# Optimization experiments

Measured on AMD Instinct MI355X. Metric: run time of the kernel, lower is better.

## Reference

```python
import jax, jax.numpy as jnp
import numpy as np

INPUT_DIM = 1024
DIM_K = 512
DIM_V = 512
N = 8192  # query rows
M = 8192  # key/value rows


def setup_inputs() -> dict:
    key = jax.random.key(0)
    ks = jax.random.split(key, 9)
    s_in = 1.0 / np.sqrt(INPUT_DIM)
    return {
        "q": jax.random.normal(ks[0], (N, INPUT_DIM), jnp.float32),
        "k": jax.random.normal(ks[1], (M, INPUT_DIM), jnp.float32),
        "v": jax.random.normal(ks[2], (M, INPUT_DIM), jnp.float32),
        "Wq": jax.random.normal(ks[3], (DIM_K, INPUT_DIM), jnp.float32) * s_in,
        "bq": jax.random.normal(ks[4], (DIM_K,), jnp.float32) * s_in,
        "Wk": jax.random.normal(ks[5], (DIM_K, INPUT_DIM), jnp.float32) * s_in,
        "bk": jax.random.normal(ks[6], (DIM_K,), jnp.float32) * s_in,
        "Wv": jax.random.normal(ks[7], (DIM_V, INPUT_DIM), jnp.float32) * s_in,
        "bv": jax.random.normal(ks[8], (DIM_V,), jnp.float32) * s_in,
    }


def reference(q, k, v, Wq, bq, Wk, bk, Wv, bv):
    norm_fact = 1.0 / np.sqrt(DIM_K).astype(np.float32)
    Q = q @ Wq.T + bq  # [N, dim_k]
    K = k @ Wk.T + bk  # [M, dim_k]
    V = v @ Wv.T + bv  # [M, dim_v]
    scores = Q @ K.T  # [N, M]
    # NOTE: faithful to source — scale is applied AFTER softmax
    atten = jax.nn.softmax(scores, axis=-1) * norm_fact
    return atten @ V  # [N, dim_v]
```

## Files before the change

### kernel.cpp

```cpp
#include <hip/hip_runtime.h>
#include <hip/hip_bf16.h>

#define IN_DIM 1024
#define DK 512
#define DV 512
#define NQ 8192
#define NKV 8192

typedef _Float16 f16x8 __attribute__((ext_vector_type(8)));
typedef _Float16 f16x4 __attribute__((ext_vector_type(4)));
typedef float f32x4 __attribute__((ext_vector_type(4)));

__global__ __launch_bounds__(256, 2) void proj_kernel(
    const float* __restrict__ qin, const float* __restrict__ kin, const float* __restrict__ vin,
    const float* __restrict__ Wq, const float* __restrict__ bq,
    const float* __restrict__ Wk, const float* __restrict__ bk,
    const float* __restrict__ Wv, const float* __restrict__ bv,
    _Float16* __restrict__ Qp, _Float16* __restrict__ Kp, _Float16* __restrict__ Vp)
{
    const int z = blockIdx.z;
    const float* A  = (z == 0) ? qin : (z == 1) ? kin : vin;
    const float* W  = (z == 0) ? Wq  : (z == 1) ? Wk  : Wv;
    const float* bi = (z == 0) ? bq  : (z == 1) ? bk  : bv;

    __shared__ __align__(16) char psm[73728];
    _Float16 (*As)[128][72] = (_Float16(*)[128][72])psm;
    _Float16 (*Bs)[128][72] = (_Float16(*)[128][72])(psm + 36864);
    _Float16* trans = (_Float16*)psm;

    const int tid = threadIdx.x;
    const int rowbase = blockIdx.y * 128;
    const int colbase = blockIdx.x * 128;
    const int wave = tid >> 6;
    const int lane = tid & 63;
    const int quad = lane >> 4;
    const int l16  = lane & 15;
    const int wrow = (wave & 1) * 64;
    const int wcol = (wave >> 1) * 64;

    float4 ra[8], rb[8];
    auto ld = [&](int kc) {
#pragma unroll
        for (int i = 0; i < 8; ++i) {
            int idx = tid + i * 256;
            int row = idx >> 4, c4 = idx & 15;
            ra[i] = *(const float4*)&A[(size_t)(rowbase + row) * IN_DIM + kc * 64 + c4 * 4];
            rb[i] = *(const float4*)&W[(size_t)(colbase + row) * IN_DIM + kc * 64 + c4 * 4];
        }
    };
    auto st = [&](int buf) {
#pragma unroll
        for (int i = 0; i < 8; ++i) {
            int idx = tid + i * 256;
            int row = idx >> 4, c4 = idx & 15;
            f16x4 pa, pb;
            pa[0] = (_Float16)ra[i].x; pa[1] = (_Float16)ra[i].y;
            pa[2] = (_Float16)ra[i].z; pa[3] = (_Float16)ra[i].w;
            pb[0] = (_Float16)rb[i].x; pb[1] = (_Float16)rb[i].y;
            pb[2] = (_Float16)rb[i].z; pb[3] = (_Float16)rb[i].w;
            *(f16x4*)&As[buf][row][c4 * 4] = pa;
            *(f16x4*)&Bs[buf][row][c4 * 4] = pb;
        }
    };

    f32x4 acc[4][4];
#pragma unroll
    for (int r = 0; r < 4; ++r)
#pragma unroll
        for (int c = 0; c < 4; ++c) acc[r][c] = (f32x4)(0.0f);

    ld(0); st(0); ld(1);
    __syncthreads();

    for (int kc = 0; kc < 16; ++kc) {
        const int buf = kc & 1;
#pragma unroll
        for (int ks = 0; ks < 2; ++ks) {
            f16x8 af[4], bfr[4];
#pragma unroll
            for (int r = 0; r < 4; ++r)
                af[r] = *(const f16x8*)&As[buf][wrow + r * 16 + l16][ks * 32 + quad * 8];
#pragma unroll
            for (int c = 0; c < 4; ++c)
                bfr[c] = *(const f16x8*)&Bs[buf][wcol + c * 16 + l16][ks * 32 + quad * 8];
#pragma unroll
            for (int r = 0; r < 4; ++r)
#pragma unroll
                for (int c = 0; c < 4; ++c)
                    acc[r][c] = __builtin_amdgcn_mfma_f32_16x16x32_f16(af[r], bfr[c], acc[r][c], 0, 0, 0);
        }
        if (kc + 1 < 16) st(buf ^ 1);
        if (kc + 2 < 16) ld(kc + 2);
        __syncthreads();
    }

    const int S = 152;
    if (z < 2) {
        _Float16* outp = (z == 0) ? Qp : Kp;
#pragma unroll
        for (int c = 0; c < 4; ++c) {
            int col = wcol + c * 16 + l16;
            float bval = bi[colbase + col];
#pragma unroll
            for (int r = 0; r < 4; ++r)
#pragma unroll
                for (int g = 0; g < 4; ++g) {
                    int row = wrow + r * 16 + quad * 4 + g;
                    trans[row * S + col] = (_Float16)(acc[r][c][g] + bval);
                }
        }
        __syncthreads();
#pragma unroll
        for (int i = 0; i < 2; ++i)
#pragma unroll
            for (int stp = 0; stp < 4; ++stp) {
                int tl = wave * 2 + i;
                f16x8 v = *(const f16x8*)&trans[(tl * 16 + l16) * S + stp * 32 + quad * 8];
                size_t fi = (size_t)((blockIdx.y * 8 + tl) * 16 + (blockIdx.x * 4 + stp));
                *(f16x8*)&outp[fi * 512 + lane * 8] = v;
            }
    } else {
#pragma unroll
        for (int c = 0; c < 4; ++c) {
            int dv = wcol + c * 16 + l16;
            float bval = bi[colbase + dv];
#pragma unroll
            for (int r = 0; r < 4; ++r)
#pragma unroll
                for (int g = 0; g < 4; ++g) {
                    int key = wrow + r * 16 + quad * 4 + g;
                    trans[dv * S + key] = (_Float16)(acc[r][c][g] + bval);
                }
        }
        __syncthreads();
#pragma unroll
        for (int i = 0; i < 2; ++i)
#pragma unroll
            for (int chl = 0; chl < 2; ++chl)
#pragma unroll
                for (int kst = 0; kst < 2; ++kst) {
                    int tdl = wave * 2 + i;
                    f16x8 v = *(const f16x8*)&trans[(tdl * 16 + l16) * S + chl * 64 + kst * 32 + quad * 8];
                    size_t fi = ((size_t)(blockIdx.y * 2 + chl) * 32 + (blockIdx.x * 8 + tdl)) * 2 + kst;
                    *(f16x8*)&Vp[fi * 512 + lane * 8] = v;
                }
    }
}

__global__ __launch_bounds__(512, 2) void flash_kernel(
    const _Float16* __restrict__ Qp, const _Float16* __restrict__ Kp,
    const _Float16* __restrict__ Vp, float* __restrict__ outp)
{
    __shared__ __align__(16) _Float16 Qls[16384];
    __shared__ __align__(16) _Float16 Ps[2][32][72];
    __shared__ float Smax2[32][12];
    __shared__ float Ssum2[32][12];
    __shared__ float lfin[32];

    const int tid  = threadIdx.x;
    const int w    = tid >> 6;
    const int lane = tid & 63;
    const int quad = lane >> 4;
    const int l16  = lane & 15;
    const int qbase = blockIdx.x * 32;

    {
        const f16x8* src = (const f16x8*)(Qp + (size_t)qbase * 512);
        f16x8* dst = (f16x8*)Qls;
#pragma unroll
        for (int i = 0; i < 4; ++i)
            dst[tid + i * 512] = src[tid + i * 512];
    }

    float mreg0 = -1e30f, mreg1 = -1e30f, lreg0 = 0.0f, lreg1 = 0.0f;
    f32x4 oacc[2][4];
#pragma unroll
    for (int qt = 0; qt < 2; ++qt)
#pragma unroll
        for (int t = 0; t < 4; ++t) oacc[qt][t] = (f32x4)(0.0f);

    const _Float16* kfp = Kp + (size_t)w * 16 * 512 + lane * 8;
    f16x8 kf[16];
#pragma unroll
    for (int stp = 0; stp < 16; ++stp)
        kf[stp] = *(const f16x8*)(kfp + (size_t)stp * 512);

    asm volatile("s_waitcnt lgkmcnt(0)" ::: "memory");
    __builtin_amdgcn_s_barrier();

    f16x8 vf[16];

    for (int ch = 0; ch < 64; ++ch) {
        const _Float16* vp = Vp + ((size_t)ch * 128 + w * 8) * 512 + lane * 8;
#pragma unroll
        for (int h = 0; h < 2; ++h)
#pragma unroll
            for (int t = 0; t < 4; ++t)
#pragma unroll
                for (int ks = 0; ks < 2; ++ks)
                    vf[h * 8 + t * 2 + ks] = *(const f16x8*)(vp + (size_t)(h * 64 + t * 2 + ks) * 512);

        f32x4 st0 = (f32x4)(0.0f), st1 = (f32x4)(0.0f);
        __builtin_amdgcn_s_setprio(1);
#pragma unroll
        for (int stp = 0; stp < 16; ++stp) {
            f16x8 q0 = *(const f16x8*)&Qls[(size_t)stp * 512 + lane * 8];
            f16x8 q1 = *(const f16x8*)&Qls[(size_t)(16 + stp) * 512 + lane * 8];
            st0 = __builtin_amdgcn_mfma_f32_16x16x32_f16(kf[stp], q0, st0, 0, 0, 0);
            st1 = __builtin_amdgcn_mfma_f32_16x16x32_f16(kf[stp], q1, st1, 0, 0, 0);
        }
        __builtin_amdgcn_s_setprio(0);

        float ms0 = fmaxf(fmaxf(st0[0], st0[1]), fmaxf(st0[2], st0[3]));
        float ms1 = fmaxf(fmaxf(st1[0], st1[1]), fmaxf(st1[2], st1[3]));
        ms0 = fmaxf(ms0, __shfl_xor(ms0, 16)); ms0 = fmaxf(ms0, __shfl_xor(ms0, 32));
        ms1 = fmaxf(ms1, __shfl_xor(ms1, 16)); ms1 = fmaxf(ms1, __shfl_xor(ms1, 32));
        if (lane < 16) { Smax2[lane][w] = ms0; Smax2[16 + lane][w] = ms1; }

        if (ch + 1 < 64) {
            const _Float16* kp = kfp + (size_t)(ch + 1) * 65536;
#pragma unroll
            for (int stp = 0; stp < 16; ++stp)
                kf[stp] = *(const f16x8*)(kp + (size_t)stp * 512);
        }

        asm volatile("s_waitcnt lgkmcnt(0)" ::: "memory");
        __builtin_amdgcn_s_barrier();

        float4 a0 = *(const float4*)&Smax2[l16][0];
        float4 b0 = *(const float4*)&Smax2[l16][4];
        float mt0 = fmaxf(fmaxf(fmaxf(a0.x, a0.y), fmaxf(a0.z, a0.w)),
                          fmaxf(fmaxf(b0.x, b0.y), fmaxf(b0.z, b0.w)));
        float4 a1 = *(const float4*)&Smax2[16 + l16][0];
        float4 b1 = *(const float4*)&Smax2[16 + l16][4];
        float mt1 = fmaxf(fmaxf(fmaxf(a1.x, a1.y), fmaxf(a1.z, a1.w)),
                          fmaxf(fmaxf(b1.x, b1.y), fmaxf(b1.z, b1.w)));
        float mn0 = fmaxf(mreg0, mt0);
        float mn1 = fmaxf(mreg1, mt1);
        float alpha0 = __expf(mreg0 - mn0); mreg0 = mn0; lreg0 *= alpha0;
        float alpha1 = __expf(mreg1 - mn1); mreg1 = mn1; lreg1 *= alpha1;

        float p00 = __expf(st0[0] - mn0), p01 = __expf(st0[1] - mn0);
        float p02 = __expf(st0[2] - mn0), p03 = __expf(st0[3] - mn0);
        float p10 = __expf(st1[0] - mn1), p11 = __expf(st1[1] - mn1);
        float p12 = __expf(st1[2] - mn1), p13 = __expf(st1[3] - mn1);
        f16x4 pp0, pp1;
        pp0[0] = (_Float16)p00; pp0[1] = (_Float16)p01;
        pp0[2] = (_Float16)p02; pp0[3] = (_Float16)p03;
        pp1[0] = (_Float16)p10; pp1[1] = (_Float16)p11;
        pp1[2] = (_Float16)p12; pp1[3] = (_Float16)p13;
        *(f16x4*)&Ps[w >> 2][l16][(w & 3) * 16 + quad * 4]      = pp0;
        *(f16x4*)&Ps[w >> 2][16 + l16][(w & 3) * 16 + quad * 4] = pp1;

        float ts0 = (p00 + p01) + (p02 + p03);
        float ts1 = (p10 + p11) + (p12 + p13);
        ts0 += __shfl_xor(ts0, 16); ts0 += __shfl_xor(ts0, 32);
        ts1 += __shfl_xor(ts1, 16); ts1 += __shfl_xor(ts1, 32);
        if (lane < 16) { Ssum2[lane][w] = ts0; Ssum2[16 + lane][w] = ts1; }

        float ao0[4], ao1[4];
#pragma unroll
        for (int g = 0; g < 4; ++g) {
            ao0[g] = __shfl(alpha0, quad * 20 + g);
            ao1[g] = __shfl(alpha1, quad * 20 + g);
        }
#pragma unroll
        for (int t = 0; t < 4; ++t)
#pragma unroll
            for (int g = 0; g < 4; ++g) {
                oacc[0][t][g] *= ao0[g];
                oacc[1][t][g] *= ao1[g];
            }

        asm volatile("s_waitcnt lgkmcnt(0)" ::: "memory");
        __builtin_amdgcn_s_barrier();

        {
            float4 sa = *(const float4*)&Ssum2[l16][0];
            float4 sb = *(const float4*)&Ssum2[l16][4];
            lreg0 += (sa.x + sa.y) + (sa.z + sa.w) + (sb.x + sb.y) + (sb.z + sb.w);
            float4 sc = *(const float4*)&Ssum2[16 + l16][0];
            float4 sd = *(const float4*)&Ssum2[16 + l16][4];
            lreg1 += (sc.x + sc.y) + (sc.z + sc.w) + (sd.x + sd.y) + (sd.z + sd.w);
        }

        __builtin_amdgcn_s_setprio(1);
#pragma unroll
        for (int kst = 0; kst < 4; ++kst) {
            f16x8 pa0 = *(const f16x8*)&Ps[kst >> 1][l16][(kst & 1) * 32 + quad * 8];
            f16x8 pa1 = *(const f16x8*)&Ps[kst >> 1][16 + l16][(kst & 1) * 32 + quad * 8];
            const int vb = (kst >> 1) * 8 + (kst & 1);
#pragma unroll
            for (int t = 0; t < 4; ++t) {
                oacc[0][t] = __builtin_amdgcn_mfma_f32_16x16x32_f16(pa0, vf[vb + t * 2], oacc[0][t], 0, 0, 0);
                oacc[1][t] = __builtin_amdgcn_mfma_f32_16x16x32_f16(pa1, vf[vb + t * 2], oacc[1][t], 0, 0, 0);
            }
        }
        __builtin_amdgcn_s_setprio(0);
    }

    if (w == 0 && lane < 16) { lfin[lane] = lreg0; lfin[16 + lane] = lreg1; }
    __syncthreads();

    const float norm = 0.044194173824159216f;
#pragma unroll
    for (int qt = 0; qt < 2; ++qt)
#pragma unroll
        for (int g = 0; g < 4; ++g) {
            const int row = qbase + qt * 16 + quad * 4 + g;
            const float sc = norm / lfin[qt * 16 + quad * 4 + g];
#pragma unroll
            for (int t = 0; t < 4; ++t)
                outp[(size_t)row * 512 + w * 64 + t * 16 + l16] = oacc[qt][t][g] * sc;
        }
}

extern "C" void kernel_launch(void* const* d_in, const int* in_sizes, int n_in,
                              void* d_out, int out_size, void* d_ws, size_t ws_size,
                              hipStream_t stream) {
    const float* q  = (const float*)d_in[0];
    const float* k  = (const float*)d_in[1];
    const float* v  = (const float*)d_in[2];
    const float* Wq = (const float*)d_in[3];
    const float* bq = (const float*)d_in[4];
    const float* Wk = (const float*)d_in[5];
    const float* bk = (const float*)d_in[6];
    const float* Wv = (const float*)d_in[7];
    const float* bv = (const float*)d_in[8];

    _Float16* Qp = (_Float16*)d_ws;
    _Float16* Kp = Qp + (size_t)NQ * DK;
    _Float16* Vp = Kp + (size_t)NKV * DK;
    float* outp = (float*)d_out;

    proj_kernel<<<dim3(DK / 128, NQ / 128, 3), 256, 0, stream>>>(
        q, k, v, Wq, bq, Wk, bk, Wv, bv, Qp, Kp, Vp);
    flash_kernel<<<dim3(NQ / 32), 512, 0, stream>>>(Qp, Kp, Vp, outp);
}
```

Before: 379.8 us.

## Use per-wave local max for softmax to drop one barrier per chunk

Each wave now exponentiates its scores against its own local row max, so it no longer waits for the block-wide max before writing P. Max and sum partials go to shared memory together, and the per-wave correction factors are computed after a single barrier. They are applied by scaling the P fragments before the PV MFMA, and the shared buffers are double-buffered by chunk parity so the next iteration's writes cannot race the current reads. This removes one of the two block barriers per KV chunk. In exchange it adds extra exponentials and packed half-precision multiplies on P, and P values rounded to fp16 relative to the local max may lose some precision.

Result: no change. 375.0 us (-1.3%).

```diff
diff --git a/kernel.cpp b/kernel.cpp
--- a/kernel.cpp
+++ b/kernel.cpp
@@ -152,9 +152,9 @@
     const _Float16* __restrict__ Vp, float* __restrict__ outp)
 {
     __shared__ __align__(16) _Float16 Qls[16384];
-    __shared__ __align__(16) _Float16 Ps[2][32][72];
-    __shared__ float Smax2[32][12];
-    __shared__ float Ssum2[32][12];
+    __shared__ __align__(16) _Float16 Ps[2][2][32][72];
+    __shared__ float Smax2[2][32][12];
+    __shared__ float Ssum2[2][32][12];
     __shared__ float lfin[32];
 
     const int tid  = threadIdx.x;
@@ -191,6 +191,8 @@
     f16x8 vf[16];
 
     for (int ch = 0; ch < 64; ++ch) {
+        const int p = ch & 1;
+
         const _Float16* vp = Vp + ((size_t)ch * 128 + w * 8) * 512 + lane * 8;
 #pragma unroll
         for (int h = 0; h < 2; ++h)
@@ -215,48 +217,68 @@
         float ms1 = fmaxf(fmaxf(st1[0], st1[1]), fmaxf(st1[2], st1[3]));
         ms0 = fmaxf(ms0, __shfl_xor(ms0, 16)); ms0 = fmaxf(ms0, __shfl_xor(ms0, 32));
         ms1 = fmaxf(ms1, __shfl_xor(ms1, 16)); ms1 = fmaxf(ms1, __shfl_xor(ms1, 32));
-        if (lane < 16) { Smax2[lane][w] = ms0; Smax2[16 + lane][w] = ms1; }
-
-        if (ch + 1 < 64) {
-            const _Float16* kp = kfp + (size_t)(ch + 1) * 65536;
-#pragma unroll
-            for (int stp = 0; stp < 16; ++stp)
-                kf[stp] = *(const f16x8*)(kp + (size_t)stp * 512);
-        }
-
-        asm volatile("s_waitcnt lgkmcnt(0)" ::: "memory");
-        __builtin_amdgcn_s_barrier();
-
-        float4 a0 = *(const float4*)&Smax2[l16][0];
-        float4 b0 = *(const float4*)&Smax2[l16][4];
-        float mt0 = fmaxf(fmaxf(fmaxf(a0.x, a0.y), fmaxf(a0.z, a0.w)),
-                          fmaxf(fmaxf(b0.x, b0.y), fmaxf(b0.z, b0.w)));
-        float4 a1 = *(const float4*)&Smax2[16 + l16][0];
-        float4 b1 = *(const float4*)&Smax2[16 + l16][4];
-        float mt1 = fmaxf(fmaxf(fmaxf(a1.x, a1.y), fmaxf(a1.z, a1.w)),
-                          fmaxf(fmaxf(b1.x, b1.y), fmaxf(b1.z, b1.w)));
-        float mn0 = fmaxf(mreg0, mt0);
-        float mn1 = fmaxf(mreg1, mt1);
-        float alpha0 = __expf(mreg0 - mn0); mreg0 = mn0; lreg0 *= alpha0;
-        float alpha1 = __expf(mreg1 - mn1); mreg1 = mn1; lreg1 *= alpha1;
-
-        float p00 = __expf(st0[0] - mn0), p01 = __expf(st0[1] - mn0);
-        float p02 = __expf(st0[2] - mn0), p03 = __expf(st0[3] - mn0);
-        float p10 = __expf(st1[0] - mn1), p11 = __expf(st1[1] - mn1);
-        float p12 = __expf(st1[2] - mn1), p13 = __expf(st1[3] - mn1);
+
+        float p00 = __expf(st0[0] - ms0), p01 = __expf(st0[1] - ms0);
+        float p02 = __expf(st0[2] - ms0), p03 = __expf(st0[3] - ms0);
+        float p10 = __expf(st1[0] - ms1), p11 = __expf(st1[1] - ms1);
+        float p12 = __expf(st1[2] - ms1), p13 = __expf(st1[3] - ms1);
         f16x4 pp0, pp1;
         pp0[0] = (_Float16)p00; pp0[1] = (_Float16)p01;
         pp0[2] = (_Float16)p02; pp0[3] = (_Float16)p03;
         pp1[0] = (_Float16)p10; pp1[1] = (_Float16)p11;
         pp1[2] = (_Float16)p12; pp1[3] = (_Float16)p13;
-        *(f16x4*)&Ps[w >> 2][l16][(w & 3) * 16 + quad * 4]      = pp0;
-        *(f16x4*)&Ps[w >> 2][16 + l16][(w & 3) * 16 + quad * 4] = pp1;
+        *(f16x4*)&Ps[p][w >> 2][l16][(w & 3) * 16 + quad * 4]      = pp0;
+        *(f16x4*)&Ps[p][w >> 2][16 + l16][(w & 3) * 16 + quad * 4] = pp1;
 
         float ts0 = (p00 + p01) + (p02 + p03);
         float ts1 = (p10 + p11) + (p12 + p13);
         ts0 += __shfl_xor(ts0, 16); ts0 += __shfl_xor(ts0, 32);
         ts1 += __shfl_xor(ts1, 16); ts1 += __shfl_xor(ts1, 32);
-        if (lane < 16) { Ssum2[lane][w] = ts0; Ssum2[16 + lane][w] = ts1; }
+        if (lane < 16) {
+            Smax2[p][lane][w] = ms0; Smax2[p][16 + lane][w] = ms1;
+            Ssum2[p][lane][w] = ts0; Ssum2[p][16 + lane][w] = ts1;
+        }
+
+        if (ch + 1 < 64) {
+            const _Float16* kp = kfp + (size_t)(ch + 1) * 65536;
+#pragma unroll
+            for (int stp = 0; stp < 16; ++stp)
+                kf[stp] = *(const f16x8*)(kp + (size_t)stp * 512);
+        }
+
+        asm volatile("s_waitcnt lgkmcnt(0)" ::: "memory");
+        __builtin_amdgcn_s_barrier();
+
+        float4 a0 = *(const float4*)&Smax2[p][l16][0];
+        float4 b0 = *(const float4*)&Smax2[p][l16][4];
+        float4 a1 = *(const float4*)&Smax2[p][16 + l16][0];
+        float4 b1 = *(const float4*)&Smax2[p][16 + l16][4];
+        float mt0 = fmaxf(fmaxf(fmaxf(a0.x, a0.y), fmaxf(a0.z, a0.w)),
+                          fmaxf(fmaxf(b0.x, b0.y), fmaxf(b0.z, b0.w)));
+        float mt1 = fmaxf(fmaxf(fmaxf(a1.x, a1.y), fmaxf(a1.z, a1.w)),
+                          fmaxf(fmaxf(b1.x, b1.y), fmaxf(b1.z, b1.w)));
+        float mn0 = fmaxf(mreg0, mt0);
+        float mn1 = fmaxf(mreg1, mt1);
+        float alpha0 = __expf(mreg0 - mn0); mreg0 = mn0;
+        float alpha1 = __expf(mreg1 - mn1); mreg1 = mn1;
+
+        float s0_0 = __expf(a0.x - mn0), s0_1 = __expf(a0.y - mn0);
+        float s0_2 = __expf(a0.z - mn0), s0_3 = __expf(a0.w - mn0);
+        float s0_4 = __expf(b0.x - mn0), s0_5 = __expf(b0.y - mn0);
+        float s0_6 = __expf(b0.z - mn0), s0_7 = __expf(b0.w - mn0);
+        float s1_0 = __expf(a1.x - mn1), s1_1 = __expf(a1.y - mn1);
+        float s1_2 = __expf(a1.z - mn1), s1_3 = __expf(a1.w - mn1);
+        float s1_4 = __expf(b1.x - mn1), s1_5 = __expf(b1.y - mn1);
+        float s1_6 = __expf(b1.z - mn1), s1_7 = __expf(b1.w - mn1);
+
+        float4 sa = *(const float4*)&Ssum2[p][l16][0];
+        float4 sb = *(const float4*)&Ssum2[p][l16][4];
+        float4 sc4 = *(const float4*)&Ssum2[p][16 + l16][0];
+        float4 sd4 = *(const float4*)&Ssum2[p][16 + l16][4];
+        lreg0 = lreg0 * alpha0 + (s0_0 * sa.x + s0_1 * sa.y + s0_2 * sa.z + s0_3 * sa.w)
+                               + (s0_4 * sb.x + s0_5 * sb.y + s0_6 * sb.z + s0_7 * sb.w);
+        lreg1 = lreg1 * alpha1 + (s1_0 * sc4.x + s1_1 * sc4.y + s1_2 * sc4.z + s1_3 * sc4.w)
+                               + (s1_4 * sd4.x + s1_5 * sd4.y + s1_6 * sd4.z + s1_7 * sd4.w);
 
         float ao0[4], ao1[4];
 #pragma unroll
@@ -272,23 +294,25 @@
                 oacc[1][t][g] *= ao1[g];
             }
 
-        asm volatile("s_waitcnt lgkmcnt(0)" ::: "memory");
-        __builtin_amdgcn_s_barrier();
-
-        {
-            float4 sa = *(const float4*)&Ssum2[l16][0];
-            float4 sb = *(const float4*)&Ssum2[l16][4];
-            lreg0 += (sa.x + sa.y) + (sa.z + sa.w) + (sb.x + sb.y) + (sb.z + sb.w);
-            float4 sc = *(const float4*)&Ssum2[16 + l16][0];
-            float4 sd = *(const float4*)&Ssum2[16 + l16][4];
-            lreg1 += (sc.x + sc.y) + (sc.z + sc.w) + (sd.x + sd.y) + (sd.z + sd.w);
-        }
+        const bool hi = (lane & 32) != 0;
+        const _Float16 c00 = (_Float16)(hi ? s0_1 : s0_0);
+        const _Float16 c01 = (_Float16)(hi ? s0_3 : s0_2);
+        const _Float16 c02 = (_Float16)(hi ? s0_5 : s0_4);
+        const _Float16 c03 = (_Float16)(hi ? s0_7 : s0_6);
+        const _Float16 c10 = (_Float16)(hi ? s1_1 : s1_0);
+        const _Float16 c11 = (_Float16)(hi ? s1_3 : s1_2);
+        const _Float16 c12 = (_Float16)(hi ? s1_5 : s1_4);
+        const _Float16 c13 = (_Float16)(hi ? s1_7 : s1_6);
 
         __builtin_amdgcn_s_setprio(1);
 #pragma unroll
         for (int kst = 0; kst < 4; ++kst) {
-            f16x8 pa0 = *(const f16x8*)&Ps[kst >> 1][l16][(kst & 1) * 32 + quad * 8];
-            f16x8 pa1 = *(const f16x8*)&Ps[kst >> 1][16 + l16][(kst & 1) * 32 + quad * 8];
+            const _Float16 sA = (kst == 0) ? c00 : (kst == 1) ? c01 : (kst == 2) ? c02 : c03;
+            const _Float16 sB = (kst == 0) ? c10 : (kst == 1) ? c11 : (kst == 2) ? c12 : c13;
+            f16x8 pa0 = *(const f16x8*)&Ps[p][kst >> 1][l16][(kst & 1) * 32 + quad * 8];
+            f16x8 pa1 = *(const f16x8*)&Ps[p][kst >> 1][16 + l16][(kst & 1) * 32 + quad * 8];
+            pa0 = pa0 * sA;
+            pa1 = pa1 * sB;
             const int vb = (kst >> 1) * 8 + (kst & 1);
 #pragma unroll
             for (int t = 0; t < 4; ++t) {
```
